# Kernel tuning notes

Hardware: AMD Instinct MI355X
Metric: run time of the kernel (lower is better)

Reference implementation:

```python
import jax, jax.numpy as jnp
import numpy as np

C = 256
H = 4  # hard-coded head count in SA_Layer reshapes
EPS = 1e-5


def _bn(x, gamma, beta):
    # training-mode BatchNorm1d over (batch, length) per channel; x: [b,c,n]
    m = jnp.mean(x, axis=(0, 2), keepdims=True)
    v = jnp.var(x, axis=(0, 2), keepdims=True)
    return gamma[None, :, None] * (x - m) * jax.lax.rsqrt(v + EPS) + beta[None, :, None]


def _conv1(w, x, b=None):
    # 1x1 Conv1d == per-point matmul; w: [o,c], x: [b,c,n]
    y = jnp.einsum('oc,bcn->bon', w, x)
    return y if b is None else y + b[None, :, None]


def _sa_layer(x, xyz_emb, qk_w, v_w, v_b, t_w, t_b, bn_g, bn_b):
    b, c, n = x.shape
    h = x + xyz_emb                      # [b,c,n]
    q = _conv1(qk_w, h)                  # [b,c,n]  (q and k share weights)
    # quirky reshape: permute to [b,n,c] then view as [b,H,n,c//H]
    x_q = jnp.transpose(q, (0, 2, 1)).reshape(b, H, n, c // H)
    x_k = q.reshape(b, H, c // H, n)     # standard channel head split
    x_v = _conv1(v_w, h, v_b).reshape(b, H, c // H, n)
    energy = jnp.matmul(x_q, x_k)        # [b,H,n,n]
    att = jax.nn.softmax(energy, axis=-1)
    att = jax.nn.softmax(att, axis=-2)   # dual softmax
    x_r = jnp.matmul(x_v, att).reshape(b, c, n)
    x_r = jax.nn.relu(_bn(_conv1(t_w, x - x_r, t_b), bn_g, bn_b))
    return x + x_r


def setup_inputs() -> dict:
    key = jax.random.key(0)
    ks = jax.random.split(key, 16)
    B, N = 4, 2048
    s = 1.0 / np.sqrt(C)
    inp = {
        'x': jax.random.normal(ks[0], (B, C, N), jnp.float32),
        'xyz': jax.random.normal(ks[1], (B, N, 3), jnp.float32),
        'conv1_w': jax.random.normal(ks[2], (C, C), jnp.float32) * s,
        'pos_w': jax.random.normal(ks[3], (C, 3), jnp.float32) * 0.5,
        'pos_b': jax.random.normal(ks[4], (C,), jnp.float32) * 0.02,
        'bn1_g': jnp.ones((C,), jnp.float32),
        'bn1_b': jnp.zeros((C,), jnp.float32),
        'qk_w': jax.random.normal(ks[5], (4, C, C), jnp.float32) * s,
        'v_w': jax.random.normal(ks[6], (4, C, C), jnp.float32) * s,
        'v_b': jax.random.normal(ks[7], (4, C), jnp.float32) * 0.02,
        't_w': jax.random.normal(ks[8], (4, C, C), jnp.float32) * s,
        't_b': jax.random.normal(ks[9], (4, C), jnp.float32) * 0.02,
        'bn_g': jnp.ones((4, C), jnp.float32),
        'bn_b': jnp.zeros((4, C), jnp.float32),
    }
    return inp


def reference(x, xyz, conv1_w, pos_w, pos_b, bn1_g, bn1_b,
              qk_w, v_w, v_b, t_w, t_b, bn_g, bn_b):
    # xyz: [B,N,3] -> permute -> pos_xyz (1x1 conv)
    xyz_emb = jnp.einsum('oi,bni->bon', pos_w, xyz) + pos_b[None, :, None]  # [b,C,n]
    h = jax.nn.relu(_bn(_conv1(conv1_w, x), bn1_g, bn1_b))
    outs = []
    for i in range(4):
        h = _sa_layer(h, xyz_emb, qk_w[i], v_w[i], v_b[i],
                      t_w[i], t_b[i], bn_g[i], bn_b[i])
        outs.append(h)
    return jnp.concatenate(outs, axis=1)  # [b, 4*C, n]
```

## Files before the change

kernel.cpp:

```cpp
#include <hip/hip_runtime.h>
#include <math.h>

#define Bsz 4
#define Cch 256
#define Npt 2048
#define Hh  4
#define NL  4
#define BN_CNT (Bsz * Npt)
#define EPSV 1e-5f
#define NROW (16 * Npt)
#define L2E 1.44269504f

typedef _Float16 f16x8 __attribute__((ext_vector_type(8)));
typedef _Float16 f16x4 __attribute__((ext_vector_type(4)));
typedef float    f32x4 __attribute__((ext_vector_type(4)));

__device__ __forceinline__ float fexp2(float x) { return __builtin_amdgcn_exp2f(x); }

__device__ __forceinline__ void gld16(const _Float16* g, _Float16* l) {
    __builtin_amdgcn_global_load_lds(
        (const __attribute__((address_space(1))) unsigned int*)g,
        (__attribute__((address_space(3))) unsigned int*)l, 16, 0, 0);
}

__global__ void k_xyz_emb(const float* __restrict__ xyz, const float* __restrict__ pw,
                          const float* __restrict__ pb, float* __restrict__ emb) {
    int idx = blockIdx.x * 256 + threadIdx.x;
    int n = idx & (Npt - 1);
    int c = (idx >> 11) & (Cch - 1);
    int b = idx >> 19;
    const float* xz = xyz + (b * Npt + n) * 3;
    emb[idx] = pw[c * 3 + 0] * xz[0] + pw[c * 3 + 1] * xz[1] + pw[c * 3 + 2] * xz[2] + pb[c];
}

__global__ void k_castw(const float* __restrict__ c1w, const float* __restrict__ qkw,
                        const float* __restrict__ vw, const float* __restrict__ tw,
                        _Float16* __restrict__ o, float* __restrict__ bnacc) {
    int i = blockIdx.x * 256 + threadIdx.x;
    if (i < 5 * 512) bnacc[i] = 0.f;
    const float* src; int off;
    if (i < 65536)            { src = c1w; off = i; }
    else if (i < 327680)      { src = qkw; off = i - 65536; }
    else if (i < 589824)      { src = vw;  off = i - 327680; }
    else                      { src = tw;  off = i - 589824; }
    o[i] = (_Float16)src[off];
}

__global__ __launch_bounds__(256) void k_fuse_t(const float* __restrict__ in,
        _Float16* __restrict__ XT) {
    __shared__ _Float16 Tt[64][72];
    const int b = blockIdx.z, c0 = blockIdx.y * 64, n0 = blockIdx.x * 64;
    const int t = threadIdx.x;
    const int cl = t >> 2, ns = (t & 3) * 16;
    const float* ip = in + ((size_t)(b * Cch + c0 + cl) * Npt) + n0 + ns;
    #pragma unroll
    for (int g = 0; g < 4; ++g) {
        float4 v = *(const float4*)(ip + g * 4);
        Tt[ns + g * 4 + 0][cl] = (_Float16)v.x;
        Tt[ns + g * 4 + 1][cl] = (_Float16)v.y;
        Tt[ns + g * 4 + 2][cl] = (_Float16)v.z;
        Tt[ns + g * 4 + 3][cl] = (_Float16)v.w;
    }
    __syncthreads();
    int nl = t >> 2, cs = (t & 3) * 16;
    _Float16* op = XT + ((size_t)(b * Npt + n0 + nl) * Cch) + c0 + cs;
    #pragma unroll
    for (int g = 0; g < 4; ++g)
        *(f16x4*)(op + g * 4) = *(f16x4*)&Tt[nl][cs + g * 4];
}

__global__ __launch_bounds__(256) void k_gemm_mfma(const _Float16* __restrict__ Wb,
        const _Float16* __restrict__ XT, const float* __restrict__ bias,
        float* __restrict__ Yf, float* __restrict__ bnacc) {
    __shared__ float EpF[64][68];
    const int b = blockIdx.z, o0 = blockIdx.y * 64, n0 = blockIdx.x * 64;
    const int tid = threadIdx.x, w = tid >> 6, quad = (tid >> 4) & 3, tx = tid & 15;
    const _Float16* Arow = Wb + (o0 + w * 16 + tx) * Cch + quad * 8;
    const _Float16* Brow = XT + ((size_t)(b * Npt + n0 + tx) * Cch) + quad * 8;
    f32x4 acc[4];
    #pragma unroll
    for (int s = 0; s < 4; ++s) acc[s] = (f32x4){0.f, 0.f, 0.f, 0.f};
    for (int k0 = 0; k0 < Cch; k0 += 32) {
        f16x8 a = *(const f16x8*)(Arow + k0);
        #pragma unroll
        for (int s = 0; s < 4; ++s) {
            f16x8 bb = *(const f16x8*)(Brow + s * 16 * Cch + k0);
            acc[s] = __builtin_amdgcn_mfma_f32_16x16x32_f16(a, bb, acc[s], 0, 0, 0);
        }
    }
    float bv[4];
    {
        int ob = o0 + w * 16 + quad * 4;
        if (bias) { bv[0] = bias[ob]; bv[1] = bias[ob + 1]; bv[2] = bias[ob + 2]; bv[3] = bias[ob + 3]; }
        else bv[0] = bv[1] = bv[2] = bv[3] = 0.f;
    }
    #pragma unroll
    for (int s = 0; s < 4; ++s) {
        int ol = w * 16 + quad * 4, nl = s * 16 + tx;
        EpF[ol + 0][nl] = acc[s][0] + bv[0];
        EpF[ol + 1][nl] = acc[s][1] + bv[1];
        EpF[ol + 2][nl] = acc[s][2] + bv[2];
        EpF[ol + 3][nl] = acc[s][3] + bv[3];
    }
    __syncthreads();
    int row = tid >> 2, seg = (tid & 3) * 16;
    float* yp = Yf + ((size_t)(b * Cch + o0 + row) * Npt) + n0 + seg;
    float s1 = 0.f, s2 = 0.f;
    #pragma unroll
    for (int g = 0; g < 4; ++g) {
        float4 v = *(float4*)&EpF[row][seg + g * 4];
        *(float4*)(yp + g * 4) = v;
        s1 += v.x + v.y + v.z + v.w;
        s2 += v.x * v.x + v.y * v.y + v.z * v.z + v.w * v.w;
    }
    s1 += __shfl_xor(s1, 1); s2 += __shfl_xor(s2, 1);
    s1 += __shfl_xor(s1, 2); s2 += __shfl_xor(s2, 2);
    if ((tid & 3) == 0) {
        atomicAdd(&bnacc[o0 + row], s1);
        atomicAdd(&bnacc[256 + o0 + row], s2);
    }
}

__global__ __launch_bounds__(256) void k_gemm_qkv(const _Float16* __restrict__ Wqk,
        const _Float16* __restrict__ Wv, const _Float16* __restrict__ XT,
        const float* __restrict__ vbias, _Float16* __restrict__ Vb,
        _Float16* __restrict__ Qg, _Float16* __restrict__ Kt) {
    __shared__ _Float16 EpB[64][72];
    const int b = blockIdx.z, y = blockIdx.y, n0 = blockIdx.x * 64;
    const int isV = (y >= 4);
    const int o0 = (isV ? (y - 4) : y) * 64;
    const _Float16* Wb = isV ? Wv : Wqk;
    const int tid = threadIdx.x, w = tid >> 6, quad = (tid >> 4) & 3, tx = tid & 15;
    const _Float16* Arow = Wb + (o0 + w * 16 + tx) * Cch + quad * 8;
    const _Float16* Brow = XT + ((size_t)(b * Npt + n0 + tx) * Cch) + quad * 8;
    f32x4 acc[4];
    #pragma unroll
    for (int s = 0; s < 4; ++s) acc[s] = (f32x4){0.f, 0.f, 0.f, 0.f};
    for (int k0 = 0; k0 < Cch; k0 += 32) {
        f16x8 a = *(const f16x8*)(Arow + k0);
        #pragma unroll
        for (int s = 0; s < 4; ++s) {
            f16x8 bb = *(const f16x8*)(Brow + s * 16 * Cch + k0);
            acc[s] = __builtin_amdgcn_mfma_f32_16x16x32_f16(a, bb, acc[s], 0, 0, 0);
        }
    }
    if (!isV) {
        const int cch = (w << 1) + (quad >> 1);
        const int hof = (quad & 1) * 4;
        #pragma unroll
        for (int s = 0; s < 4; ++s) {
            int ng = n0 + s * 16 + tx;
            f16x4 pk;
            pk[0] = (_Float16)acc[s][0]; pk[1] = (_Float16)acc[s][1];
            pk[2] = (_Float16)acc[s][2]; pk[3] = (_Float16)acc[s][3];
            int rK = ng & 63, jt = ng >> 6;
            size_t ka = ((size_t)((b * Hh + (o0 >> 6)) * 32 + jt) << 12)
                      + rK * 64 + ((cch ^ (rK & 7)) * 8) + hof;
            *(f16x4*)&Kt[ka] = pk;
            int iQ = ((ng & 511) << 2) + (o0 >> 6);
            int rQ = iQ & 63, it = iQ >> 6;
            size_t qa = ((size_t)((b * Hh + (ng >> 9)) * 32 + it) << 12)
                      + rQ * 64 + ((cch ^ (rQ & 7)) * 8) + hof;
            *(f16x4*)&Qg[qa] = pk;
        }
        return;
    }
    float bv[4];
    {
        int ob = o0 + w * 16 + quad * 4;
        bv[0] = vbias[ob]; bv[1] = vbias[ob + 1]; bv[2] = vbias[ob + 2]; bv[3] = vbias[ob + 3];
    }
    #pragma unroll
    for (int s = 0; s < 4; ++s) {
        int ol = w * 16 + quad * 4, nl = s * 16 + tx;
        EpB[ol + 0][nl] = (_Float16)(acc[s][0] + bv[0]);
        EpB[ol + 1][nl] = (_Float16)(acc[s][1] + bv[1]);
        EpB[ol + 2][nl] = (_Float16)(acc[s][2] + bv[2]);
        EpB[ol + 3][nl] = (_Float16)(acc[s][3] + bv[3]);
    }
    __syncthreads();
    int row = tid >> 2, seg = (tid & 3) * 16;
    _Float16* yp = Vb + ((size_t)(b * Cch + o0 + row) * Npt) + n0 + seg;
    #pragma unroll
    for (int g = 0; g < 4; ++g)
        *(f16x4*)(yp + g * 4) = *(f16x4*)&EpB[row][seg + g * 4];
}

__global__ __launch_bounds__(256) void k_attn_A(const _Float16* __restrict__ Qg,
        const _Float16* __restrict__ Kt, float* __restrict__ mP, float* __restrict__ lP) {
    __shared__ _Float16 Ksh[2][4096];
    const int flat = blockIdx.x;
    const int bh = (flat & 7) * 2 + ((flat >> 3) & 1);
    const int rest = flat >> 4;
    const int i0 = (rest & 15) * 128;
    const int jc = rest >> 4;
    const int tid = threadIdx.x, w = tid >> 6, q = (tid >> 4) & 3, tx = tid & 15;
    const int lane = tid & 63;
    const int sx = tx & 7;
    f16x8 qa[2][2];
    #pragma unroll
    for (int g = 0; g < 2; ++g) {
        const _Float16* Qtile = Qg + ((size_t)(bh * 32 + ((i0 + g * 64) >> 6)) << 12);
        int r = w * 16 + tx;
        qa[g][0] = *(const f16x8*)(Qtile + r * 64 + (q ^ sx) * 8);
        qa[g][1] = *(const f16x8*)(Qtile + r * 64 + ((q + 4) ^ sx) * 8);
    }
    const _Float16* Kbase = Kt + ((size_t)(bh * 32) << 12);
    const int jt0 = jc * 8;
    {
        const _Float16* g = Kbase + ((size_t)jt0 << 12) + (w * 2) * 512 + lane * 8;
        gld16(g,       &Ksh[0][(w * 2 + 0) * 512]);
        gld16(g + 512, &Ksh[0][(w * 2 + 1) * 512]);
    }
    __syncthreads();
    float m2[2][4], l[2][4];
    #pragma unroll
    for (int g = 0; g < 2; ++g)
        #pragma unroll
        for (int r = 0; r < 4; ++r) { m2[g][r] = -1e30f; l[g][r] = 0.f; }
    for (int t = 0; t < 8; ++t) {
        if (t < 7) {
            const _Float16* g = Kbase + ((size_t)(jt0 + t + 1) << 12) + (w * 2) * 512 + lane * 8;
            gld16(g,       &Ksh[(t + 1) & 1][(w * 2 + 0) * 512]);
            gld16(g + 512, &Ksh[(t + 1) & 1][(w * 2 + 1) * 512]);
        }
        const _Float16* kbuf = Ksh[t & 1];
        f32x4 e[2][4];
        #pragma unroll
        for (int s = 0; s < 4; ++s) {
            int r = s * 16 + tx;
            f16x8 kb0 = *(const f16x8*)(kbuf + r * 64 + (q ^ sx) * 8);
            f16x8 kb1 = *(const f16x8*)(kbuf + r * 64 + ((q + 4) ^ sx) * 8);
            #pragma unroll
            for (int g = 0; g < 2; ++g) {
                f32x4 z = (f32x4){0.f, 0.f, 0.f, 0.f};
                z = __builtin_amdgcn_mfma_f32_16x16x32_f16(qa[g][0], kb0, z, 0, 0, 0);
                e[g][s] = __builtin_amdgcn_mfma_f32_16x16x32_f16(qa[g][1], kb1, z, 0, 0, 0);
            }
        }
        #pragma unroll
        for (int g = 0; g < 2; ++g)
            #pragma unroll
            for (int r = 0; r < 4; ++r) {
                float e0 = e[g][0][r] * L2E, e1 = e[g][1][r] * L2E;
                float e2 = e[g][2][r] * L2E, e3 = e[g][3][r] * L2E;
                float lm = fmaxf(fmaxf(e0, e1), fmaxf(e2, e3));
                float nm = fmaxf(m2[g][r], lm);
                l[g][r] = l[g][r] * fexp2(m2[g][r] - nm)
                        + fexp2(e0 - nm) + fexp2(e1 - nm) + fexp2(e2 - nm) + fexp2(e3 - nm);
                m2[g][r] = nm;
            }
        __syncthreads();
    }
    #pragma unroll
    for (int g = 0; g < 2; ++g)
        #pragma unroll
        for (int r = 0; r < 4; ++r) {
            float mm = m2[g][r], ll = l[g][r];
            #pragma unroll
            for (int off = 1; off < 16; off <<= 1) {
                float om = __shfl_xor(mm, off), ol = __shfl_xor(ll, off);
                float nm = fmaxf(mm, om);
                ll = ll * fexp2(mm - nm) + ol * fexp2(om - nm);
                mm = nm;
            }
            if (tx == 0) {
                int idx = bh * Npt + i0 + g * 64 + w * 16 + q * 4 + r;
                mP[jc * NROW + idx] = mm;
                lP[jc * NROW + idx] = ll;
            }
        }
}

__global__ __launch_bounds__(256) void k_attn_B(const _Float16* __restrict__ Qg,
        const _Float16* __restrict__ Kt, const _Float16* __restrict__ Vb,
        const float* __restrict__ mP, const float* __restrict__ lP,
        const float* __restrict__ h, _Float16* __restrict__ XT) {
    __shared__ _Float16 AtT[4][2048];
    __shared__ float mlm[Npt];
    __shared__ float mll[Npt];
    __shared__ float Ssh[4][32];
    __shared__ float rsv[32];
    const int flat = blockIdx.x;
    const int bh = (flat & 7) * 2 + ((flat >> 3) & 1);
    const int j0 = (flat >> 4) * 32;
    const int b = bh >> 2, hd = bh & 3;
    const int tid = threadIdx.x, w = tid >> 6, q = (tid >> 4) & 3, tx = tid & 15;
    const int sx = tx & 7;
    {
        const int ib = tid * 8;
        #pragma unroll
        for (int e = 0; e < 2; ++e) {
            int ii = ib + e * 4;
            int idx = bh * Npt + ii;
            float4 m0 = *(const float4*)&mP[idx];
            float4 m1 = *(const float4*)&mP[NROW + idx];
            float4 m2 = *(const float4*)&mP[2 * NROW + idx];
            float4 m3 = *(const float4*)&mP[3 * NROW + idx];
            float4 l0 = *(const float4*)&lP[idx];
            float4 l1 = *(const float4*)&lP[NROW + idx];
            float4 l2 = *(const float4*)&lP[2 * NROW + idx];
            float4 l3 = *(const float4*)&lP[3 * NROW + idx];
            #pragma unroll
            for (int k = 0; k < 4; ++k) {
                float a0 = ((const float*)&m0)[k], a1 = ((const float*)&m1)[k];
                float a2 = ((const float*)&m2)[k], a3 = ((const float*)&m3)[k];
                float mm = fmaxf(fmaxf(a0, a1), fmaxf(a2, a3));
                float ll = ((const float*)&l0)[k] * fexp2(a0 - mm)
                         + ((const float*)&l1)[k] * fexp2(a1 - mm)
                         + ((const float*)&l2)[k] * fexp2(a2 - mm)
                         + ((const float*)&l3)[k] * fexp2(a3 - mm);
                mlm[ii + k] = mm;
                mll[ii + k] = L2E / ll;
            }
        }
    }
    __syncthreads();
    f16x8 kb[2][2];
    const _Float16* Ktile = Kt + ((size_t)(bh * 32 + (j0 >> 6)) << 12);
    const int jb = j0 & 32;
    #pragma unroll
    for (int nt = 0; nt < 2; ++nt) {
        int r = jb + nt * 16 + tx;
        kb[nt][0] = *(const f16x8*)(Ktile + r * 64 + (q ^ sx) * 8);
        kb[nt][1] = *(const f16x8*)(Ktile + r * 64 + ((q + 4) ^ sx) * 8);
    }
    f32x4 Tacc[4][2];
    #pragma unroll
    for (int mt = 0; mt < 4; ++mt)
        #pragma unroll
        for (int nt = 0; nt < 2; ++nt) Tacc[mt][nt] = (f32x4){0.f, 0.f, 0.f, 0.f};
    float scS[2] = {0.f, 0.f};
    _Float16* myAt = AtT[w];
    const _Float16* vbase = Vb + (size_t)(b * Cch + hd * 64) * Npt;
    for (int it = 0; it < 8; ++it) {
        const int i0 = w * 512 + it * 64;
        const _Float16* Qtile = Qg + ((size_t)(bh * 32 + (i0 >> 6)) << 12);
        #pragma unroll
        for (int mt = 0; mt < 4; ++mt) {
            int r = mt * 16 + tx;
            f16x8 qa0 = *(const f16x8*)(Qtile + r * 64 + (q ^ sx) * 8);
            f16x8 qa1 = *(const f16x8*)(Qtile + r * 64 + ((q + 4) ^ sx) * 8);
            float4 m2v = *(const float4*)&mlm[i0 + mt * 16 + q * 4];
            float4 liv = *(const float4*)&mll[i0 + mt * 16 + q * 4];
            #pragma unroll
            for (int nt = 0; nt < 2; ++nt) {
                f32x4 z = (f32x4){0.f, 0.f, 0.f, 0.f};
                z = __builtin_amdgcn_mfma_f32_16x16x32_f16(qa0, kb[nt][0], z, 0, 0, 0);
                z = __builtin_amdgcn_mfma_f32_16x16x32_f16(qa1, kb[nt][1], z, 0, 0, 0);
                float a0 = fexp2(fexp2(__builtin_fmaf(z[0], L2E, -m2v.x)) * liv.x);
                float a1 = fexp2(fexp2(__builtin_fmaf(z[1], L2E, -m2v.y)) * liv.y);
                float a2 = fexp2(fexp2(__builtin_fmaf(z[2], L2E, -m2v.z)) * liv.z);
                float a3 = fexp2(fexp2(__builtin_fmaf(z[3], L2E, -m2v.w)) * liv.w);
                scS[nt] += a0 + a1 + a2 + a3;
                f16x4 pk;
                pk[0] = (_Float16)a0; pk[1] = (_Float16)a1;
                pk[2] = (_Float16)a2; pk[3] = (_Float16)a3;
                *(f16x4*)&myAt[(nt * 16 + tx) * 64 + ((2 * mt + (q >> 1)) ^ sx) * 8 + (q & 1) * 4] = pk;
            }
        }
        f16x8 pb[2][2], va[4][2];
        #pragma unroll
        for (int nt = 0; nt < 2; ++nt) {
            int r = nt * 16 + tx;
            pb[nt][0] = *(const f16x8*)&myAt[r * 64 + (q ^ sx) * 8];
            pb[nt][1] = *(const f16x8*)&myAt[r * 64 + ((q + 4) ^ sx) * 8];
        }
        #pragma unroll
        for (int mt = 0; mt < 4; ++mt) {
            const _Float16* vp = vbase + (size_t)(mt * 16 + tx) * Npt + i0 + q * 8;
            va[mt][0] = *(const f16x8*)(vp);
            va[mt][1] = *(const f16x8*)(vp + 32);
        }
        #pragma unroll
        for (int mt = 0; mt < 4; ++mt)
            #pragma unroll
            for (int nt = 0; nt < 2; ++nt) {
                Tacc[mt][nt] = __builtin_amdgcn_mfma_f32_16x16x32_f16(va[mt][0], pb[nt][0], Tacc[mt][nt], 0, 0, 0);
                Tacc[mt][nt] = __builtin_amdgcn_mfma_f32_16x16x32_f16(va[mt][1], pb[nt][1], Tacc[mt][nt], 0, 0, 0);
            }
    }
    #pragma unroll
    for (int mt = 0; mt < 4; ++mt)
        #pragma unroll
        for (int nt = 0; nt < 2; ++nt) {
            f16x4 pk;
            pk[0] = (_Float16)Tacc[mt][nt][0];
            pk[1] = (_Float16)Tacc[mt][nt][1];
            pk[2] = (_Float16)Tacc[mt][nt][2];
            pk[3] = (_Float16)Tacc[mt][nt][3];
            *(f16x4*)&myAt[(nt * 16 + tx) * 64 + ((2 * mt + (q >> 1)) ^ sx) * 8 + (q & 1) * 4] = pk;
        }
    #pragma unroll
    for (int nt = 0; nt < 2; ++nt) {
        float s = scS[nt];
        s += __shfl_xor(s, 16);
        s += __shfl_xor(s, 32);
        if (q == 0) Ssh[w][nt * 16 + tx] = s;
    }
    __syncthreads();
    if (tid < 32)
        rsv[tid] = 1.f / (Ssh[0][tid] + Ssh[1][tid] + Ssh[2][tid] + Ssh[3][tid]);
    __syncthreads();
    {
        const int jl = tid >> 3, half = tid & 7;
        const int slot = ((half ^ (jl & 7)) * 8);
        const int base = jl * 64 + slot;
        f16x8 t0 = *(const f16x8*)&AtT[0][base];
        f16x8 t1 = *(const f16x8*)&AtT[1][base];
        f16x8 t2 = *(const f16x8*)&AtT[2][base];
        f16x8 t3 = *(const f16x8*)&AtT[3][base];
        const float rs = rsv[jl];
        const float* hp = h + ((size_t)(b * Cch + hd * 64 + half * 8) * Npt) + j0 + jl;
        f16x8 u;
        #pragma unroll
        for (int e = 0; e < 8; ++e) {
            float tv = (float)t0[e] + (float)t1[e] + (float)t2[e] + (float)t3[e];
            u[e] = (_Float16)(hp[(size_t)e * Npt] - tv * rs);
        }
        *(f16x8*)(XT + ((size_t)(b * Npt + j0 + jl) * Cch) + hd * 64 + half * 8) = u;
    }
}

__global__ __launch_bounds__(256) void k_bn_fuse(const float* __restrict__ t,
        const float* __restrict__ bnacc,
        const float* __restrict__ g, const float* __restrict__ bt,
        const float* __restrict__ emb, const float* __restrict__ resid,
        float* __restrict__ hout, float* __restrict__ out, _Float16* __restrict__ XT,
        int layer) {
    __shared__ _Float16 Tt[64][72];
    const int b = blockIdx.z, c0 = blockIdx.y * 64, n0 = blockIdx.x * 64;
    const int tt = threadIdx.x;
    const int cl = tt >> 2, ns = (tt & 3) * 16;
    const int c = c0 + cl;
    const float mn = bnacc[c] * (1.f / BN_CNT);
    const float var = bnacc[256 + c] * (1.f / BN_CNT) - mn * mn;
    const float is = rsqrtf(var + EPSV);
    const float gg = g[c], bb = bt[c];
    const size_t rowoff = ((size_t)(b * Cch + c) * Npt) + n0 + ns;
    const float* tp = t + rowoff;
    const float* ep = emb + rowoff;
    const float* rp = resid ? resid + rowoff : nullptr;
    float* hp = hout + rowoff;
    float* op = out ? out + (size_t)b * (NL * Cch * Npt) + (size_t)(layer * Cch + c) * Npt + n0 + ns
                    : nullptr;
    #pragma unroll
    for (int gi = 0; gi < 4; ++gi) {
        float4 v = *(const float4*)(tp + gi * 4);
        float4 y;
        y.x = fmaxf(gg * (v.x - mn) * is + bb, 0.f);
        y.y = fmaxf(gg * (v.y - mn) * is + bb, 0.f);
        y.z = fmaxf(gg * (v.z - mn) * is + bb, 0.f);
        y.w = fmaxf(gg * (v.w - mn) * is + bb, 0.f);
        if (rp) {
            float4 r = *(const float4*)(rp + gi * 4);
            y.x += r.x; y.y += r.y; y.z += r.z; y.w += r.w;
        }
        *(float4*)(hp + gi * 4) = y;
        if (op) *(float4*)(op + gi * 4) = y;
        float4 e = *(const float4*)(ep + gi * 4);
        Tt[ns + gi * 4 + 0][cl] = (_Float16)(y.x + e.x);
        Tt[ns + gi * 4 + 1][cl] = (_Float16)(y.y + e.y);
        Tt[ns + gi * 4 + 2][cl] = (_Float16)(y.z + e.z);
        Tt[ns + gi * 4 + 3][cl] = (_Float16)(y.w + e.w);
    }
    __syncthreads();
    int nl = tt >> 2, cs = (tt & 3) * 16;
    _Float16* xp = XT + ((size_t)(b * Npt + n0 + nl) * Cch) + c0 + cs;
    #pragma unroll
    for (int gi = 0; gi < 4; ++gi)
        *(f16x4*)(xp + gi * 4) = *(f16x4*)&Tt[nl][cs + gi * 4];
}

extern "C" void kernel_launch(void* const* d_in, const int* in_sizes, int n_in,
                              void* d_out, int out_size, void* d_ws, size_t ws_size,
                              hipStream_t stream) {
    (void)in_sizes; (void)n_in; (void)out_size; (void)ws_size;
    const float* x    = (const float*)d_in[0];
    const float* xyz  = (const float*)d_in[1];
    const float* c1w  = (const float*)d_in[2];
    const float* posw = (const float*)d_in[3];
    const float* posb = (const float*)d_in[4];
    const float* bn1g = (const float*)d_in[5];
    const float* bn1b = (const float*)d_in[6];
    const float* qkw  = (const float*)d_in[7];
    const float* vw   = (const float*)d_in[8];
    const float* vb   = (const float*)d_in[9];
    const float* tw   = (const float*)d_in[10];
    const float* tb   = (const float*)d_in[11];
    const float* bng  = (const float*)d_in[12];
    const float* bnb  = (const float*)d_in[13];
    float* out = (float*)d_out;

    const size_t NE = (size_t)Bsz * Cch * Npt;
    char* W = (char*)d_ws;
    float* emb   = (float*)W;                 W += NE * 4;
    float* h     = (float*)W;                 W += NE * 4;
    float* vbuf  = (float*)W;                 W += NE * 4;
    _Float16* XT = (_Float16*)W;              W += NE * 2;
    _Float16* Qg = (_Float16*)W;              W += NE * 2;
    _Float16* Kt = (_Float16*)W;              W += NE * 2;
    _Float16* Vb = (_Float16*)W;              W += NE * 2;
    _Float16* wbf = (_Float16*)W;             W += 851968 * 2;
    float* mP    = (float*)W;                 W += 4 * NROW * 4;
    float* lP    = (float*)W;                 W += 4 * NROW * 4;
    float* bnacc = (float*)W;                 W += 5 * 512 * 4;

    dim3 blk(256);
    dim3 g4(Npt / 64, Cch / 64, Bsz);
    dim3 gQKV(Npt / 64, 8, Bsz);
    int ew = (int)(NE / 256);

    k_castw<<<3328, blk, 0, stream>>>(c1w, qkw, vw, tw, wbf, bnacc);
    k_xyz_emb<<<ew, blk, 0, stream>>>(xyz, posw, posb, emb);

    k_fuse_t<<<g4, blk, 0, stream>>>(x, XT);
    k_gemm_mfma<<<g4, blk, 0, stream>>>(wbf, XT, nullptr, vbuf, bnacc);
    k_bn_fuse<<<g4, blk, 0, stream>>>(vbuf, bnacc, bn1g, bn1b, emb, nullptr,
                                      h, nullptr, XT, 0);

    for (int L = 0; L < NL; ++L) {
        const _Float16* qkL = wbf + 65536 + (size_t)L * 65536;
        const _Float16* vL  = wbf + 327680 + (size_t)L * 65536;
        const _Float16* tL  = wbf + 589824 + (size_t)L * 65536;
        float* accL = bnacc + (1 + L) * 512;
        k_gemm_qkv<<<gQKV, blk, 0, stream>>>(qkL, vL, XT, vb + L * Cch, Vb, Qg, Kt);
        k_attn_A<<<1024, blk, 0, stream>>>(Qg, Kt, mP, lP);
        k_attn_B<<<1024, blk, 0, stream>>>(Qg, Kt, Vb, mP, lP, h, XT);
        k_gemm_mfma<<<g4, blk, 0, stream>>>(tL, XT, tb + L * Cch, vbuf, accL);
        k_bn_fuse<<<g4, blk, 0, stream>>>(vbuf, accL, bng + L * Cch, bnb + L * Cch,
                                          emb, h, h, out, XT, L);
    }
}
```

Before: 634.2 us.

## Keep attention probabilities in registers and widen attn_B blocks to 64 columns

k_attn_B now feeds the probability fragments straight from registers into the PV MFMA as the B operand. This removes the per-iteration LDS round trip, relying on a V-side column permutation that the QKV GEMM epilogue now writes in permuted order. Blocks grow to 512 threads covering 64 key columns, with two groups of 4 waves. This halves the grid and shares the mP/lP softmax-stat merge across twice as many columns. LDS use rises to 8 TS buffers, and the new launch bounds may constrain registers.

```diff
diff --git a/kernel.cpp b/kernel.cpp
--- a/kernel.cpp
+++ b/kernel.cpp
@@ -180,10 +180,12 @@
     }
     __syncthreads();
     int row = tid >> 2, seg = (tid & 3) * 16;
-    _Float16* yp = Vb + ((size_t)(b * Cch + o0 + row) * Npt) + n0 + seg;
+    const int m = tid & 3;
+    const int pbase = (m >> 1) * 32 + (m & 1) * 4;
+    _Float16* yp = Vb + ((size_t)(b * Cch + o0 + row) * Npt) + n0 + pbase;
     #pragma unroll
     for (int g = 0; g < 4; ++g)
-        *(f16x4*)(yp + g * 4) = *(f16x4*)&EpB[row][seg + g * 4];
+        *(f16x4*)(yp + g * 8) = *(f16x4*)&EpB[row][seg + g * 4];
 }
 
 __global__ __launch_bounds__(256) void k_attn_A(const _Float16* __restrict__ Qg,
@@ -272,125 +274,105 @@
         }
 }
 
-__global__ __launch_bounds__(256) void k_attn_B(const _Float16* __restrict__ Qg,
+__global__ __launch_bounds__(512, 4) void k_attn_B(const _Float16* __restrict__ Qg,
         const _Float16* __restrict__ Kt, const _Float16* __restrict__ Vb,
         const float* __restrict__ mP, const float* __restrict__ lP,
         const float* __restrict__ h, _Float16* __restrict__ XT) {
-    __shared__ _Float16 AtT[4][2048];
     __shared__ float mlm[Npt];
     __shared__ float mll[Npt];
-    __shared__ float Ssh[4][32];
-    __shared__ float rsv[32];
+    __shared__ float Ssh[8][32];
+    __shared__ _Float16 TS[8][2048];
     const int flat = blockIdx.x;
     const int bh = (flat & 7) * 2 + ((flat >> 3) & 1);
-    const int j0 = (flat >> 4) * 32;
+    const int j0 = (flat >> 4) * 64;
     const int b = bh >> 2, hd = bh & 3;
     const int tid = threadIdx.x, w = tid >> 6, q = (tid >> 4) & 3, tx = tid & 15;
     const int sx = tx & 7;
+    const int jh = w >> 2;
+    const int wq = w & 3;
     {
-        const int ib = tid * 8;
-        #pragma unroll
-        for (int e = 0; e < 2; ++e) {
-            int ii = ib + e * 4;
-            int idx = bh * Npt + ii;
-            float4 m0 = *(const float4*)&mP[idx];
-            float4 m1 = *(const float4*)&mP[NROW + idx];
-            float4 m2 = *(const float4*)&mP[2 * NROW + idx];
-            float4 m3 = *(const float4*)&mP[3 * NROW + idx];
-            float4 l0 = *(const float4*)&lP[idx];
-            float4 l1 = *(const float4*)&lP[NROW + idx];
-            float4 l2 = *(const float4*)&lP[2 * NROW + idx];
-            float4 l3 = *(const float4*)&lP[3 * NROW + idx];
-            #pragma unroll
-            for (int k = 0; k < 4; ++k) {
-                float a0 = ((const float*)&m0)[k], a1 = ((const float*)&m1)[k];
-                float a2 = ((const float*)&m2)[k], a3 = ((const float*)&m3)[k];
-                float mm = fmaxf(fmaxf(a0, a1), fmaxf(a2, a3));
-                float ll = ((const float*)&l0)[k] * fexp2(a0 - mm)
-                         + ((const float*)&l1)[k] * fexp2(a1 - mm)
-                         + ((const float*)&l2)[k] * fexp2(a2 - mm)
-                         + ((const float*)&l3)[k] * fexp2(a3 - mm);
-                mlm[ii + k] = mm;
-                mll[ii + k] = L2E / ll;
-            }
-        }
-    }
-    __syncthreads();
+        const int ii = tid * 4;
+        const int idx = bh * Npt + ii;
+        float4 m0 = *(const float4*)&mP[idx];
+        float4 m1 = *(const float4*)&mP[NROW + idx];
+        float4 m2 = *(const float4*)&mP[2 * NROW + idx];
+        float4 m3 = *(const float4*)&mP[3 * NROW + idx];
+        float4 l0 = *(const float4*)&lP[idx];
+        float4 l1 = *(const float4*)&lP[NROW + idx];
+        float4 l2 = *(const float4*)&lP[2 * NROW + idx];
+        float4 l3 = *(const float4*)&lP[3 * NROW + idx];
+        #pragma unroll
+        for (int k = 0; k < 4; ++k) {
+            float a0 = ((const float*)&m0)[k], a1 = ((const float*)&m1)[k];
+            float a2 = ((const float*)&m2)[k], a3 = ((const float*)&m3)[k];
+            float mm = fmaxf(fmaxf(a0, a1), fmaxf(a2, a3));
+            float ll = ((const float*)&l0)[k] * fexp2(a0 - mm)
+                     + ((const float*)&l1)[k] * fexp2(a1 - mm)
+                     + ((const float*)&l2)[k] * fexp2(a2 - mm)
+                     + ((const float*)&l3)[k] * fexp2(a3 - mm);
+            mlm[ii + k] = mm;
+            mll[ii + k] = L2E / ll;
+        }
+    }
     f16x8 kb[2][2];
-    const _Float16* Ktile = Kt + ((size_t)(bh * 32 + (j0 >> 6)) << 12);
-    const int jb = j0 & 32;
-    #pragma unroll
-    for (int nt = 0; nt < 2; ++nt) {
-        int r = jb + nt * 16 + tx;
-        kb[nt][0] = *(const f16x8*)(Ktile + r * 64 + (q ^ sx) * 8);
-        kb[nt][1] = *(const f16x8*)(Ktile + r * 64 + ((q + 4) ^ sx) * 8);
-    }
+    {
+        const _Float16* Ktile = Kt + ((size_t)(bh * 32 + (j0 >> 6)) << 12);
+        #pragma unroll
+        for (int nt = 0; nt < 2; ++nt) {
+            int r = jh * 32 + nt * 16 + tx;
+            kb[nt][0] = *(const f16x8*)(Ktile + r * 64 + (q ^ sx) * 8);
+            kb[nt][1] = *(const f16x8*)(Ktile + r * 64 + ((q + 4) ^ sx) * 8);
+        }
+    }
+    __syncthreads();
     f32x4 Tacc[4][2];
     #pragma unroll
     for (int mt = 0; mt < 4; ++mt)
         #pragma unroll
         for (int nt = 0; nt < 2; ++nt) Tacc[mt][nt] = (f32x4){0.f, 0.f, 0.f, 0.f};
     float scS[2] = {0.f, 0.f};
-    _Float16* myAt = AtT[w];
     const _Float16* vbase = Vb + (size_t)(b * Cch + hd * 64) * Npt;
     for (int it = 0; it < 8; ++it) {
-        const int i0 = w * 512 + it * 64;
+        const int i0 = wq * 512 + it * 64;
         const _Float16* Qtile = Qg + ((size_t)(bh * 32 + (i0 >> 6)) << 12);
         #pragma unroll
-        for (int mt = 0; mt < 4; ++mt) {
-            int r = mt * 16 + tx;
-            f16x8 qa0 = *(const f16x8*)(Qtile + r * 64 + (q ^ sx) * 8);
-            f16x8 qa1 = *(const f16x8*)(Qtile + r * 64 + ((q + 4) ^ sx) * 8);
-            float4 m2v = *(const float4*)&mlm[i0 + mt * 16 + q * 4];
-            float4 liv = *(const float4*)&mll[i0 + mt * 16 + q * 4];
+        for (int pp = 0; pp < 2; ++pp) {
+            f16x4 pk[2][2];
             #pragma unroll
-            for (int nt = 0; nt < 2; ++nt) {
-                f32x4 z = (f32x4){0.f, 0.f, 0.f, 0.f};
-                z = __builtin_amdgcn_mfma_f32_16x16x32_f16(qa0, kb[nt][0], z, 0, 0, 0);
-                z = __builtin_amdgcn_mfma_f32_16x16x32_f16(qa1, kb[nt][1], z, 0, 0, 0);
-                float a0 = fexp2(fexp2(__builtin_fmaf(z[0], L2E, -m2v.x)) * liv.x);
-                float a1 = fexp2(fexp2(__builtin_fmaf(z[1], L2E, -m2v.y)) * liv.y);
-                float a2 = fexp2(fexp2(__builtin_fmaf(z[2], L2E, -m2v.z)) * liv.z);
-                float a3 = fexp2(fexp2(__builtin_fmaf(z[3], L2E, -m2v.w)) * liv.w);
-                scS[nt] += a0 + a1 + a2 + a3;
-                f16x4 pk;
-                pk[0] = (_Float16)a0; pk[1] = (_Float16)a1;
-                pk[2] = (_Float16)a2; pk[3] = (_Float16)a3;
-                *(f16x4*)&myAt[(nt * 16 + tx) * 64 + ((2 * mt + (q >> 1)) ^ sx) * 8 + (q & 1) * 4] = pk;
+            for (int mt2 = 0; mt2 < 2; ++mt2) {
+                const int mt = pp * 2 + mt2;
+                const int r = mt * 16 + tx;
+                f16x8 qa0 = *(const f16x8*)(Qtile + r * 64 + (q ^ sx) * 8);
+                f16x8 qa1 = *(const f16x8*)(Qtile + r * 64 + ((q + 4) ^ sx) * 8);
+                float4 m2v = *(const float4*)&mlm[i0 + mt * 16 + q * 4];
+                float4 liv = *(const float4*)&mll[i0 + mt * 16 + q * 4];
+                #pragma unroll
+                for (int nt = 0; nt < 2; ++nt) {
+                    f32x4 z = (f32x4){0.f, 0.f, 0.f, 0.f};
+                    z = __builtin_amdgcn_mfma_f32_16x16x32_f16(qa0, kb[nt][0], z, 0, 0, 0);
+                    z = __builtin_amdgcn_mfma_f32_16x16x32_f16(qa1, kb[nt][1], z, 0, 0, 0);
+                    float a0 = fexp2(fexp2(__builtin_fmaf(z[0], L2E, -m2v.x)) * liv.x);
+                    float a1 = fexp2(fexp2(__builtin_fmaf(z[1], L2E, -m2v.y)) * liv.y);
+                    float a2 = fexp2(fexp2(__builtin_fmaf(z[2], L2E, -m2v.z)) * liv.z);
+                    float a3 = fexp2(fexp2(__builtin_fmaf(z[3], L2E, -m2v.w)) * liv.w);
+                    scS[nt] += a0 + a1 + a2 + a3;
+                    f16x4 pkk;
+                    pkk[0] = (_Float16)a0; pkk[1] = (_Float16)a1;
+                    pkk[2] = (_Float16)a2; pkk[3] = (_Float16)a3;
+                    pk[mt2][nt] = pkk;
+                }
             }
-        }
-        f16x8 pb[2][2], va[4][2];
-        #pragma unroll
-        for (int nt = 0; nt < 2; ++nt) {
-            int r = nt * 16 + tx;
-            pb[nt][0] = *(const f16x8*)&myAt[r * 64 + (q ^ sx) * 8];
-            pb[nt][1] = *(const f16x8*)&myAt[r * 64 + ((q + 4) ^ sx) * 8];
-        }
-        #pragma unroll
-        for (int mt = 0; mt < 4; ++mt) {
-            const _Float16* vp = vbase + (size_t)(mt * 16 + tx) * Npt + i0 + q * 8;
-            va[mt][0] = *(const f16x8*)(vp);
-            va[mt][1] = *(const f16x8*)(vp + 32);
-        }
-        #pragma unroll
-        for (int mt = 0; mt < 4; ++mt)
             #pragma unroll
-            for (int nt = 0; nt < 2; ++nt) {
-                Tacc[mt][nt] = __builtin_amdgcn_mfma_f32_16x16x32_f16(va[mt][0], pb[nt][0], Tacc[mt][nt], 0, 0, 0);
-                Tacc[mt][nt] = __builtin_amdgcn_mfma_f32_16x16x32_f16(va[mt][1], pb[nt][1], Tacc[mt][nt], 0, 0, 0);
+            for (int mtd = 0; mtd < 4; ++mtd) {
+                f16x8 va = *(const f16x8*)(vbase + (size_t)(mtd * 16 + tx) * Npt + i0 + pp * 32 + q * 8);
+                #pragma unroll
+                for (int nt = 0; nt < 2; ++nt) {
+                    f16x8 pb = __builtin_shufflevector(pk[0][nt], pk[1][nt], 0, 1, 2, 3, 4, 5, 6, 7);
+                    Tacc[mtd][nt] = __builtin_amdgcn_mfma_f32_16x16x32_f16(va, pb, Tacc[mtd][nt], 0, 0, 0);
+                }
             }
-    }
-    #pragma unroll
-    for (int mt = 0; mt < 4; ++mt)
-        #pragma unroll
-        for (int nt = 0; nt < 2; ++nt) {
-            f16x4 pk;
-            pk[0] = (_Float16)Tacc[mt][nt][0];
-            pk[1] = (_Float16)Tacc[mt][nt][1];
-            pk[2] = (_Float16)Tacc[mt][nt][2];
-            pk[3] = (_Float16)Tacc[mt][nt][3];
-            *(f16x4*)&myAt[(nt * 16 + tx) * 64 + ((2 * mt + (q >> 1)) ^ sx) * 8 + (q & 1) * 4] = pk;
-        }
+        }
+    }
     #pragma unroll
     for (int nt = 0; nt < 2; ++nt) {
         float s = scS[nt];
@@ -398,27 +380,38 @@
         s += __shfl_xor(s, 32);
         if (q == 0) Ssh[w][nt * 16 + tx] = s;
     }
-    __syncthreads();
-    if (tid < 32)
-        rsv[tid] = 1.f / (Ssh[0][tid] + Ssh[1][tid] + Ssh[2][tid] + Ssh[3][tid]);
+    #pragma unroll
+    for (int mtd = 0; mtd < 4; ++mtd)
+        #pragma unroll
+        for (int nt = 0; nt < 2; ++nt) {
+            f16x4 pkk;
+            pkk[0] = (_Float16)Tacc[mtd][nt][0];
+            pkk[1] = (_Float16)Tacc[mtd][nt][1];
+            pkk[2] = (_Float16)Tacc[mtd][nt][2];
+            pkk[3] = (_Float16)Tacc[mtd][nt][3];
+            *(f16x4*)&TS[w][(nt * 16 + tx) * 64 + ((2 * mtd + (q >> 1)) ^ sx) * 8 + (q & 1) * 4] = pkk;
+        }
     __syncthreads();
     {
-        const int jl = tid >> 3, half = tid & 7;
-        const int slot = ((half ^ (jl & 7)) * 8);
-        const int base = jl * 64 + slot;
-        f16x8 t0 = *(const f16x8*)&AtT[0][base];
-        f16x8 t1 = *(const f16x8*)&AtT[1][base];
-        f16x8 t2 = *(const f16x8*)&AtT[2][base];
-        f16x8 t3 = *(const f16x8*)&AtT[3][base];
-        const float rs = rsv[jl];
-        const float* hp = h + ((size_t)(b * Cch + hd * 64 + half * 8) * Npt) + j0 + jl;
+        const int jl = tid >> 3, d8 = tid & 7;
+        const int wb = (jl >> 5) * 4;
+        const int jj = jl & 31;
+        const int tsbase = jj * 64 + ((d8 ^ (jj & 7)) * 8);
+        f16x8 t0 = *(const f16x8*)&TS[wb + 0][tsbase];
+        f16x8 t1 = *(const f16x8*)&TS[wb + 1][tsbase];
+        f16x8 t2 = *(const f16x8*)&TS[wb + 2][tsbase];
+        f16x8 t3 = *(const f16x8*)&TS[wb + 3][tsbase];
+        const float s4 = Ssh[wb + 0][jj] + Ssh[wb + 1][jj] + Ssh[wb + 2][jj] + Ssh[wb + 3][jj];
+        const float rs = 1.f / s4;
+        const int jg = j0 + jl;
+        const float* hp = h + ((size_t)(b * Cch + hd * 64 + d8 * 8) * Npt) + jg;
         f16x8 u;
         #pragma unroll
         for (int e = 0; e < 8; ++e) {
             float tv = (float)t0[e] + (float)t1[e] + (float)t2[e] + (float)t3[e];
             u[e] = (_Float16)(hp[(size_t)e * Npt] - tv * rs);
         }
-        *(f16x8*)(XT + ((size_t)(b * Npt + j0 + jl) * Cch) + hd * 64 + half * 8) = u;
+        *(f16x8*)(XT + ((size_t)(b * Npt + jg) * Cch) + hd * 64 + d8 * 8) = u;
     }
 }
 
@@ -526,7 +519,7 @@
         float* accL = bnacc + (1 + L) * 512;
         k_gemm_qkv<<<gQKV, blk, 0, stream>>>(qkL, vL, XT, vb + L * Cch, Vb, Qg, Kt);
         k_attn_A<<<1024, blk, 0, stream>>>(Qg, Kt, mP, lP);
-        k_attn_B<<<1024, blk, 0, stream>>>(Qg, Kt, Vb, mP, lP, h, XT);
+        k_attn_B<<<512, dim3(512), 0, stream>>>(Qg, Kt, Vb, mP, lP, h, XT);
         k_gemm_mfma<<<g4, blk, 0, stream>>>(tL, XT, tb + L * Cch, vbuf, accL);
         k_bn_fuse<<<g4, blk, 0, stream>>>(vbuf, accL, bng + L * Cch, bnb + L * Cch,
                                           emb, h, h, out, XT, L);
```

Result: faster. 615.3 us (-3.0%).
